# Kernel optimization log

Hardware: AMD Instinct MI355X
Metric: run time of the kernel (lower is better)

The kernel has to match this reference:

```python
import jax, jax.numpy as jnp
import numpy as np

N = 100000        # nodes
E = 3200000       # random edges (avg degree 32); self-loops added in reference
IN, HID, HEADS, OUT = 10, 32, 2, 4
NEG_SLOPE = 0.2   # PyG GATConv default leaky_relu slope


def setup_inputs() -> dict:
    key = jax.random.key(0)
    ks = jax.random.split(key, 16)
    s = 0.1
    return {
        "x": jax.random.normal(ks[0], (N, IN), jnp.float32),
        "edge_index": jax.random.randint(ks[1], (2, E), 0, N),
        "W1": jax.random.normal(ks[2], (IN, HEADS * HID), jnp.float32) * s,
        "a1s": jax.random.normal(ks[3], (HEADS, HID), jnp.float32) * s,
        "a1d": jax.random.normal(ks[4], (HEADS, HID), jnp.float32) * s,
        "b1": jnp.zeros((HEADS * HID,), jnp.float32),
        "W2": jax.random.normal(ks[5], (HEADS * HID, HEADS * HID), jnp.float32) * s,
        "a2s": jax.random.normal(ks[6], (HEADS, HID), jnp.float32) * s,
        "a2d": jax.random.normal(ks[7], (HEADS, HID), jnp.float32) * s,
        "b2": jnp.zeros((HEADS * HID,), jnp.float32),
        "W3": jax.random.normal(ks[8], (HEADS * HID, OUT), jnp.float32) * s,
        "a3s": jax.random.normal(ks[9], (1, OUT), jnp.float32) * s,
        "a3d": jax.random.normal(ks[10], (1, OUT), jnp.float32) * s,
        "b3": jnp.zeros((OUT,), jnp.float32),
    }


def gat_layer(x, src, dst, W, a_src, a_dst, b, concat):
    """One PyG-style GATConv (shared src/dst linear, self-loops already in src/dst)."""
    heads, oc = a_src.shape
    h = (x @ W).reshape(-1, heads, oc)                    # [N, H, C]
    asc = jnp.einsum('nhc,hc->nh', h, a_src)              # [N, H]
    adc = jnp.einsum('nhc,hc->nh', h, a_dst)              # [N, H]
    e = jax.nn.leaky_relu(asc[src] + adc[dst], NEG_SLOPE) # [Etot, H]
    m = jax.ops.segment_max(e, dst, num_segments=N)       # segment softmax over dst
    ex = jnp.exp(e - m[dst])
    z = jax.ops.segment_sum(ex, dst, num_segments=N)
    alpha = ex / z[dst]                                   # [Etot, H]
    out = jax.ops.segment_sum(h[src] * alpha[:, :, None], dst, num_segments=N)
    out = out.reshape(-1, heads * oc) if concat else out.mean(axis=1)
    return out + b


def reference(x, edge_index, W1, a1s, a1d, b1, W2, a2s, a2d, b2, W3, a3s, a3d, b3):
    loops = jnp.arange(N)
    src = jnp.concatenate([edge_index[0], loops])
    dst = jnp.concatenate([edge_index[1], loops])
    h = jax.nn.relu(gat_layer(x, src, dst, W1, a1s, a1d, b1, True))
    h = jax.nn.relu(gat_layer(h, src, dst, W2, a2s, a2d, b2, True))
    h = gat_layer(h, src, dst, W3, a3s, a3d, b3, False)
    return jax.nn.sigmoid(h) * 100.0
```

## Files before the change

kernel.cpp:

```cpp
#include <hip/hip_runtime.h>
#include <hip/hip_bf16.h>
#include <math.h>

#define NEG_SLOPE 0.2f
#define PSHIFT 8
#define PSIZE 256
#define NPARTS_MAX 392
#define B1 768
#define CELL_CAP 32
#define PCAP 10240
#define LCSR_CAP 10240

typedef int vint2 __attribute__((ext_vector_type(2)));
typedef int vint4 __attribute__((ext_vector_type(4)));
typedef short bf16x8 __attribute__((ext_vector_type(8)));
typedef float floatx4 __attribute__((ext_vector_type(4)));

__device__ __forceinline__ float lrelu(float v) { return fmaxf(v, NEG_SLOPE * v); }

__device__ __forceinline__ unsigned short f2bf(float f) {
    unsigned int b = __float_as_uint(f);
    b += 0x7fffu + ((b >> 16) & 1u);
    return (unsigned short)(b >> 16);
}

__global__ void k_part(const int* __restrict__ src, const int* __restrict__ dst, int E,
                       int* __restrict__ pairs, int* __restrict__ ptot, int nparts) {
    __shared__ int stage[NPARTS_MAX * CELL_CAP];
    __shared__ int lcnt[NPARTS_MAX];
    int tid = threadIdx.x, blk = blockIdx.x;
    for (int i = tid; i < nparts; i += 256) lcnt[i] = 0;
    __syncthreads();
    int per = ((E + B1 * 4 - 1) / (B1 * 4)) * 4;
    int s = blk * per, e = min(E, s + per);
    bool al = ((E & 3) == 0);
    for (int i0 = s + tid * 4; i0 < e; i0 += 1024) {
        int dv[4], sv[4], nv;
        if (al && i0 + 4 <= e) {
            vint4 d4 = __builtin_nontemporal_load((const vint4*)(dst + i0));
            vint4 s4 = __builtin_nontemporal_load((const vint4*)(src + i0));
            dv[0] = d4.x; dv[1] = d4.y; dv[2] = d4.z; dv[3] = d4.w;
            sv[0] = s4.x; sv[1] = s4.y; sv[2] = s4.z; sv[3] = s4.w;
            nv = 4;
        } else {
            nv = min(4, e - i0);
            for (int k = 0; k < nv; ++k) {
                dv[k] = __builtin_nontemporal_load(dst + i0 + k);
                sv[k] = __builtin_nontemporal_load(src + i0 + k);
            }
        }
        for (int k = 0; k < nv; ++k) {
            int p = dv[k] >> PSHIFT;
            int pos = atomicAdd(&lcnt[p], 1);
            if (pos < CELL_CAP)
                stage[p * CELL_CAP + pos] = (sv[k] << PSHIFT) | (dv[k] & (PSIZE - 1));
        }
    }
    __syncthreads();
    for (int p = tid; p < nparts; p += 256) {
        int tgt = min(lcnt[p], CELL_CAP);
        if (tgt == 0) continue;
        int base = atomicAdd(&ptot[p], tgt);
        if (base + tgt > PCAP) tgt = max(0, PCAP - base);
        int* gp = pairs + (size_t)p * PCAP + base;
        const int* sp = &stage[p * CELL_CAP];
        for (int j = 0; j < tgt; ++j) gp[j] = sp[j];
    }
}

__global__ void k_pscan(const int* __restrict__ ptot, int* __restrict__ pbase,
                        int* __restrict__ row, int nparts, int N) {
    __shared__ int sh[512];
    int tid = threadIdx.x;
    int v = (tid < nparts) ? min(ptot[tid], PCAP) : 0;
    sh[tid] = v;
    __syncthreads();
    for (int off = 1; off < 512; off <<= 1) {
        int t = (tid >= off) ? sh[tid - off] : 0;
        __syncthreads();
        sh[tid] += t;
        __syncthreads();
    }
    if (tid < nparts) pbase[tid] = sh[tid] - v;
    if (tid == nparts - 1) row[N] = sh[tid];
}

__global__ void k_scat2(const int* __restrict__ pairs, const int* __restrict__ ptot,
                        const int* __restrict__ pbase, int* __restrict__ row,
                        int* __restrict__ csr, int N) {
    __shared__ int lcsr[LCSR_CAP];
    __shared__ int lhist[PSIZE], lcur[PSIZE];
    int part = blockIdx.x;
    int lo = part << PSHIFT;
    int npart = min(PSIZE, N - lo);
    int tid = threadIdx.x;
    int cnt = min(ptot[part], PCAP);
    const int* seg = pairs + (size_t)part * PCAP;
    for (int i = tid; i < PSIZE; i += 1024) lhist[i] = 0;
    __syncthreads();
    for (int i = tid; i < cnt; i += 1024)
        atomicAdd(&lhist[__builtin_nontemporal_load(&seg[i]) & (PSIZE - 1)], 1);
    __syncthreads();
    if (tid < PSIZE) lcur[tid] = lhist[tid];
    __syncthreads();
    for (int off = 1; off < PSIZE; off <<= 1) {
        int t = 0;
        if (tid < PSIZE && tid >= off) t = lcur[tid - off];
        __syncthreads();
        if (tid < PSIZE) lcur[tid] += t;
        __syncthreads();
    }
    int pb = pbase[part];
    if (tid < npart) row[lo + tid] = pb + lcur[tid] - lhist[tid];
    if (tid < PSIZE) lcur[tid] -= lhist[tid];
    __syncthreads();
    for (int i = tid; i < cnt; i += 1024) {
        int v = __builtin_nontemporal_load(&seg[i]);
        int pos = atomicAdd(&lcur[v & (PSIZE - 1)], 1);
        if (pos < LCSR_CAP) lcsr[pos] = (unsigned)v >> PSHIFT;
    }
    __syncthreads();
    for (int i = tid; i < cnt; i += 1024)
        csr[pb + i] = lcsr[i];
}

__global__ void k_lin1(const float* __restrict__ x, const float* __restrict__ W,
                       const float* __restrict__ as_, const float* __restrict__ ad_,
                       unsigned short* __restrict__ hb, float* __restrict__ asc,
                       float* __restrict__ adc, int N) {
    __shared__ float sW[10 * 64];
    int tid = threadIdx.x;
    for (int i = tid; i < 640; i += 256) sW[i] = W[i];
    __syncthreads();
    int wid = tid >> 6, lane = tid & 63;
    int n = blockIdx.x * 4 + wid;
    if (n >= N) return;
    float acc = 0.f;
#pragma unroll
    for (int k = 0; k < 10; ++k) acc += x[n * 10 + k] * sW[k * 64 + lane];
    hb[(size_t)n * 64 + lane] = f2bf(acc);
    int head = lane >> 5, cc = lane & 31;
    float rs = acc * as_[lane];
    float rd = acc * ad_[lane];
#pragma unroll
    for (int m = 16; m >= 1; m >>= 1) {
        rs += __shfl_xor(rs, m, 64);
        rd += __shfl_xor(rd, m, 64);
    }
    if (cc == 0) { asc[n * 2 + head] = rs; adc[n * 2 + head] = rd; }
}

__global__ void k_lin2(const float* __restrict__ yin, const float* __restrict__ W,
                       const float* __restrict__ as_, const float* __restrict__ ad_,
                       unsigned short* __restrict__ hb, float* __restrict__ asc,
                       float* __restrict__ adc, int N) {
    __shared__ unsigned short sW[64 * 64];
    int tid = threadIdx.x;
    for (int i = tid; i < 4096; i += 256) sW[i] = f2bf(W[i]);
    __syncthreads();
    int wid = tid >> 6, lane = tid & 63;
    int quad = lane >> 4, col = lane & 15;
    bf16x8 bfr[4][2];
#pragma unroll
    for (int blk = 0; blk < 4; ++blk)
#pragma unroll
        for (int kh = 0; kh < 2; ++kh)
#pragma unroll
            for (int j = 0; j < 8; ++j)
                bfr[blk][kh][j] = (short)sW[(kh * 32 + quad * 8 + j) * 64 + blk * 16 + col];
    float asv[4], adv[4];
#pragma unroll
    for (int blk = 0; blk < 4; ++blk) {
        asv[blk] = as_[blk * 16 + col];
        adv[blk] = ad_[blk * 16 + col];
    }
    int tile = blockIdx.x * 4 + wid;
    int nb = tile * 16;
    if (nb >= N) return;
    int mrow = nb + col; if (mrow >= N) mrow = N - 1;
    const float* yr = yin + (size_t)mrow * 64;
    bf16x8 afr[2];
#pragma unroll
    for (int kh = 0; kh < 2; ++kh) {
        const float4* p = (const float4*)(yr + kh * 32 + quad * 8);
        float4 u0 = p[0], u1 = p[1];
        afr[kh][0] = (short)f2bf(u0.x); afr[kh][1] = (short)f2bf(u0.y);
        afr[kh][2] = (short)f2bf(u0.z); afr[kh][3] = (short)f2bf(u0.w);
        afr[kh][4] = (short)f2bf(u1.x); afr[kh][5] = (short)f2bf(u1.y);
        afr[kh][6] = (short)f2bf(u1.z); afr[kh][7] = (short)f2bf(u1.w);
    }
    floatx4 acc[4];
#pragma unroll
    for (int blk = 0; blk < 4; ++blk) {
        acc[blk][0] = 0.f; acc[blk][1] = 0.f; acc[blk][2] = 0.f; acc[blk][3] = 0.f;
        acc[blk] = __builtin_amdgcn_mfma_f32_16x16x32_bf16(afr[0], bfr[blk][0], acc[blk], 0, 0, 0);
        acc[blk] = __builtin_amdgcn_mfma_f32_16x16x32_bf16(afr[1], bfr[blk][1], acc[blk], 0, 0, 0);
    }
#pragma unroll
    for (int r = 0; r < 4; ++r) {
        int m = nb + quad * 4 + r;
        if (m < N) {
#pragma unroll
            for (int blk = 0; blk < 4; ++blk)
                hb[(size_t)m * 64 + blk * 16 + col] = f2bf(acc[blk][r]);
        }
    }
    float s0[4], s1[4], d0[4], d1[4];
#pragma unroll
    for (int r = 0; r < 4; ++r) {
        s0[r] = acc[0][r] * asv[0] + acc[1][r] * asv[1];
        s1[r] = acc[2][r] * asv[2] + acc[3][r] * asv[3];
        d0[r] = acc[0][r] * adv[0] + acc[1][r] * adv[1];
        d1[r] = acc[2][r] * adv[2] + acc[3][r] * adv[3];
    }
#pragma unroll
    for (int mask = 8; mask >= 1; mask >>= 1) {
#pragma unroll
        for (int r = 0; r < 4; ++r) {
            s0[r] += __shfl_xor(s0[r], mask, 64);
            s1[r] += __shfl_xor(s1[r], mask, 64);
            d0[r] += __shfl_xor(d0[r], mask, 64);
            d1[r] += __shfl_xor(d1[r], mask, 64);
        }
    }
    if (col < 4) {
        int m = nb + quad * 4 + col;
        if (m < N) {
            float vs0 = col == 0 ? s0[0] : col == 1 ? s0[1] : col == 2 ? s0[2] : s0[3];
            float vs1 = col == 0 ? s1[0] : col == 1 ? s1[1] : col == 2 ? s1[2] : s1[3];
            float vd0 = col == 0 ? d0[0] : col == 1 ? d0[1] : col == 2 ? d0[2] : d0[3];
            float vd1 = col == 0 ? d1[0] : col == 1 ? d1[1] : col == 2 ? d1[2] : d1[3];
            asc[m * 2 + 0] = vs0; asc[m * 2 + 1] = vs1;
            adc[m * 2 + 0] = vd0; adc[m * 2 + 1] = vd1;
        }
    }
}

__global__ void k_agg(const unsigned short* __restrict__ hb, const float* __restrict__ asc,
                      const float* __restrict__ adc, const int* __restrict__ row,
                      const int* __restrict__ csr_src, const float* __restrict__ bias,
                      float* __restrict__ yout, int N, int do_relu) {
    __shared__ vint2 tbl[4][64];
    int tid = threadIdx.x;
    int wid = tid >> 6, lane = tid & 63;
    int n = blockIdx.x * 4 + wid;
    if (n >= N) return;
    int s = row[n], e = row[n + 1];
    int chq = lane & 15;
    int hq = chq >> 3;
    int jo = lane >> 4;
    float2 ad = ((const float2*)adc)[n];
    float2 asf = ((const float2*)asc)[n];
    float p_self0 = __expf(lrelu(asf.x + ad.x));
    float p_self1 = __expf(lrelu(asf.y + ad.y));
    float z0a = (lane == 0) ? p_self0 : 0.f;
    float z1a = (lane == 0) ? p_self1 : 0.f;
    float a0 = 0.f, a1 = 0.f, a2 = 0.f, a3 = 0.f;
    const char* hbase = (const char*)hb;
    int choff = chq << 3;
    for (int base = s; base < e; base += 32) {
        int cnt = e - base; if (cnt > 32) cnt = 32;
        if (lane < 32) {
            int idx = base + lane;
            int srcv = 0;
            float p0 = 0.f, p1 = 0.f;
            if (idx < e) {
                srcv = csr_src[idx];
                float2 av = ((const float2*)asc)[srcv];
                p0 = __expf(lrelu(av.x + ad.x));
                p1 = __expf(lrelu(av.y + ad.y));
            }
            z0a += p0; z1a += p1;
            int boff = srcv << 7;
            vint2 e0; e0.x = boff; e0.y = __float_as_int(p0);
            vint2 e1; e1.x = boff; e1.y = __float_as_int(p1);
            tbl[wid][lane] = e0;
            tbl[wid][32 + lane] = e1;
        }
        __builtin_amdgcn_wave_barrier();
        int tb = hq << 5;
#pragma unroll 4
        for (int j = jo; j < cnt; j += 4) {
            vint2 t = tbl[wid][tb | j];
            vint2 pk = *(const vint2*)(hbase + (unsigned)t.x + choff);
            float p = __int_as_float(t.y);
            unsigned int pa = (unsigned int)pk.x, pb = (unsigned int)pk.y;
            a0 += p * __uint_as_float(pa << 16);
            a1 += p * __uint_as_float(pa & 0xffff0000u);
            a2 += p * __uint_as_float(pb << 16);
            a3 += p * __uint_as_float(pb & 0xffff0000u);
        }
        __builtin_amdgcn_wave_barrier();
    }
    a0 += __shfl_xor(a0, 16, 64); a1 += __shfl_xor(a1, 16, 64);
    a2 += __shfl_xor(a2, 16, 64); a3 += __shfl_xor(a3, 16, 64);
    a0 += __shfl_xor(a0, 32, 64); a1 += __shfl_xor(a1, 32, 64);
    a2 += __shfl_xor(a2, 32, 64); a3 += __shfl_xor(a3, 32, 64);
#pragma unroll
    for (int msk = 16; msk >= 1; msk >>= 1) {
        z0a += __shfl_xor(z0a, msk, 64);
        z1a += __shfl_xor(z1a, msk, 64);
    }
    z0a += __shfl_xor(z0a, 32, 64);
    z1a += __shfl_xor(z1a, 32, 64);
    float zneed = hq ? z1a : z0a;
    float p_self_my = hq ? p_self1 : p_self0;
    vint2 pks = *(const vint2*)(hbase + ((unsigned)n << 7) + choff);
    unsigned int sa = (unsigned int)pks.x, sb = (unsigned int)pks.y;
    a0 += p_self_my * __uint_as_float(sa << 16);
    a1 += p_self_my * __uint_as_float(sa & 0xffff0000u);
    a2 += p_self_my * __uint_as_float(sb << 16);
    a3 += p_self_my * __uint_as_float(sb & 0xffff0000u);
    float inv = 1.f / zneed;
    float4 bv = ((const float4*)bias)[chq];
    float y0 = a0 * inv + bv.x;
    float y1 = a1 * inv + bv.y;
    float y2 = a2 * inv + bv.z;
    float y3 = a3 * inv + bv.w;
    if (do_relu) {
        y0 = fmaxf(y0, 0.f); y1 = fmaxf(y1, 0.f);
        y2 = fmaxf(y2, 0.f); y3 = fmaxf(y3, 0.f);
    }
    if (lane < 16) {
        float4 o; o.x = y0; o.y = y1; o.z = y2; o.w = y3;
        ((float4*)yout)[(size_t)n * 16 + chq] = o;
    }
}

__global__ void k_lin3(const float* __restrict__ yin, const float* __restrict__ W3,
                       const float* __restrict__ a3s, const float* __restrict__ a3d,
                       float4* __restrict__ rec, int N) {
    __shared__ float sW[256];
    int tid = threadIdx.x;
    sW[tid] = W3[tid];
    __syncthreads();
    int t = blockIdx.x * 256 + tid;
    int n = t >> 2, c = t & 3;
    if (n >= N) return;
    float acc = 0.f;
#pragma unroll
    for (int k = 0; k < 64; ++k) acc += yin[(size_t)n * 64 + k] * sW[k * 4 + c];
    float rs = acc * a3s[c], rd = acc * a3d[c];
    rs += __shfl_xor(rs, 1, 64); rs += __shfl_xor(rs, 2, 64);
    rd += __shfl_xor(rd, 1, 64); rd += __shfl_xor(rd, 2, 64);
    float a_1 = __shfl_xor(acc, 1, 64);
    float a_2 = __shfl_xor(acc, 2, 64);
    float a_3 = __shfl_xor(acc, 3, 64);
    if (c == 0) {
        unsigned int lo = (unsigned int)f2bf(acc) | ((unsigned int)f2bf(a_1) << 16);
        unsigned int hi = (unsigned int)f2bf(a_2) | ((unsigned int)f2bf(a_3) << 16);
        float4 r;
        r.x = __uint_as_float(lo); r.y = __uint_as_float(hi);
        r.z = rs; r.w = rd;
        rec[n] = r;
    }
}

__global__ void k_agg3(const float4* __restrict__ rec, const int* __restrict__ row,
                       const int* __restrict__ csr_src, const float* __restrict__ b3,
                       float* __restrict__ out, int N) {
    int tid = threadIdx.x;
    int wid = tid >> 6, lane = tid & 63;
    int n = blockIdx.x * 4 + wid;
    if (n >= N) return;
    int s = row[n], e = row[n + 1];
    float4 rn = rec[n];
    float adcn = rn.w;
    float n0 = 0.f, n1 = 0.f, n2 = 0.f, n3 = 0.f, den = 0.f;
    if (lane == 0) {
        float p = __expf(lrelu(rn.z + adcn));
        unsigned int lo = __float_as_uint(rn.x), hi = __float_as_uint(rn.y);
        n0 = p * __uint_as_float(lo << 16);
        n1 = p * __uint_as_float(lo & 0xffff0000u);
        n2 = p * __uint_as_float(hi << 16);
        n3 = p * __uint_as_float(hi & 0xffff0000u);
        den = p;
    }
    for (int idx = s + lane; idx < e; idx += 64) {
        int src = csr_src[idx];
        float4 r = rec[src];
        float p = __expf(lrelu(r.z + adcn));
        unsigned int lo = __float_as_uint(r.x), hi = __float_as_uint(r.y);
        n0 += p * __uint_as_float(lo << 16);
        n1 += p * __uint_as_float(lo & 0xffff0000u);
        n2 += p * __uint_as_float(hi << 16);
        n3 += p * __uint_as_float(hi & 0xffff0000u);
        den += p;
    }
#pragma unroll
    for (int msk = 32; msk >= 1; msk >>= 1) {
        n0 += __shfl_xor(n0, msk, 64);
        n1 += __shfl_xor(n1, msk, 64);
        n2 += __shfl_xor(n2, msk, 64);
        n3 += __shfl_xor(n3, msk, 64);
        den += __shfl_xor(den, msk, 64);
    }
    if (lane < 4) {
        float num = lane == 0 ? n0 : lane == 1 ? n1 : lane == 2 ? n2 : n3;
        float v = num / den + b3[lane];
        out[n * 4 + lane] = 100.f / (1.f + __expf(-v));
    }
}

extern "C" void kernel_launch(void* const* d_in, const int* in_sizes, int n_in,
                              void* d_out, int out_size, void* d_ws, size_t ws_size,
                              hipStream_t stream) {
    const float* x   = (const float*)d_in[0];
    const int*   ei  = (const int*)d_in[1];
    const float* W1  = (const float*)d_in[2];
    const float* a1s = (const float*)d_in[3];
    const float* a1d = (const float*)d_in[4];
    const float* b1  = (const float*)d_in[5];
    const float* W2  = (const float*)d_in[6];
    const float* a2s = (const float*)d_in[7];
    const float* a2d = (const float*)d_in[8];
    const float* b2  = (const float*)d_in[9];
    const float* W3  = (const float*)d_in[10];
    const float* a3s = (const float*)d_in[11];
    const float* a3d = (const float*)d_in[12];
    const float* b3  = (const float*)d_in[13];
    float* out = (float*)d_out;

    const int N = in_sizes[0] / 10;
    const int E = in_sizes[1] / 2;
    const int* esrc = ei;
    const int* edst = ei + E;
    const int nparts = (N + PSIZE - 1) >> PSHIFT;

    char* ws = (char*)d_ws;
    size_t off = 0;
    auto alloc = [&](size_t bytes) {
        void* p = ws + off;
        off = (off + bytes + 255) & ~(size_t)255;
        return p;
    };
    int*   row   = (int*)alloc((size_t)(N + 1) * sizeof(int));
    int*   ptot  = (int*)alloc(NPARTS_MAX * sizeof(int));
    int*   pbase = (int*)alloc(NPARTS_MAX * sizeof(int));
    int*   csr   = (int*)alloc((size_t)E * sizeof(int));
    unsigned short* hb = (unsigned short*)alloc((size_t)N * 64 * sizeof(unsigned short));
    float* y     = (float*)alloc((size_t)N * 64 * sizeof(float));
    float4* rec  = (float4*)alloc((size_t)N * sizeof(float4));
    float* asc   = (float*)alloc((size_t)N * 2 * sizeof(float));
    float* adc   = (float*)alloc((size_t)N * 2 * sizeof(float));
    int* pairs = (int*)hb;

    (void)hipMemsetAsync(ptot, 0, NPARTS_MAX * sizeof(int), stream);

    const int nw = (N + 3) / 4;
    const int tiles = (N + 15) / 16;

    k_part<<<B1, 256, 0, stream>>>(esrc, edst, E, pairs, ptot, nparts);
    k_pscan<<<1, 512, 0, stream>>>(ptot, pbase, row, nparts, N);
    k_scat2<<<nparts, 1024, 0, stream>>>(pairs, ptot, pbase, row, csr, N);

    k_lin1<<<nw, 256, 0, stream>>>(x, W1, a1s, a1d, hb, asc, adc, N);
    k_agg<<<nw, 256, 0, stream>>>(hb, asc, adc, row, csr, b1, y, N, 1);
    k_lin2<<<(tiles + 3) / 4, 256, 0, stream>>>(y, W2, a2s, a2d, hb, asc, adc, N);
    k_agg<<<nw, 256, 0, stream>>>(hb, asc, adc, row, csr, b2, y, N, 1);
    k_lin3<<<(N * 4 + 255) / 256, 256, 0, stream>>>(y, W3, a3s, a3d, rec, N);
    k_agg3<<<nw, 256, 0, stream>>>(rec, row, csr, b3, out, N);
}
```

Before: 362.8 us.

## Fuse partition with layer-1 linear, inline prefix scan, widen agg loads

Merges the edge-partitioning pass and the layer-1 linear transform into one launch by giving extra blocks the linear work. The partition staging buffer moves from hb to y so the two can run together. The separate partition prefix-scan kernel is removed; every scatter block now recomputes the 512-entry scan redundantly. The aggregation kernel now has each lane load 16 bytes (8 bf16 channels) per neighbor with 8 edges in flight instead of 4, which cuts launch count and per-edge instruction overhead but raises register use.

```diff
diff --git a/kernel.cpp b/kernel.cpp
--- a/kernel.cpp
+++ b/kernel.cpp
@@ -24,77 +24,98 @@
     return (unsigned short)(b >> 16);
 }
 
-__global__ void k_part(const int* __restrict__ src, const int* __restrict__ dst, int E,
-                       int* __restrict__ pairs, int* __restrict__ ptot, int nparts) {
-    __shared__ int stage[NPARTS_MAX * CELL_CAP];
+__global__ void k_build(const int* __restrict__ src, const int* __restrict__ dst, int E,
+                        int* __restrict__ pairs, int* __restrict__ ptot, int nparts,
+                        const float* __restrict__ x, const float* __restrict__ W,
+                        const float* __restrict__ as_, const float* __restrict__ ad_,
+                        unsigned short* __restrict__ hb, float* __restrict__ asc,
+                        float* __restrict__ adc, int N) {
+    __shared__ int shmem[NPARTS_MAX * CELL_CAP];
     __shared__ int lcnt[NPARTS_MAX];
-    int tid = threadIdx.x, blk = blockIdx.x;
-    for (int i = tid; i < nparts; i += 256) lcnt[i] = 0;
-    __syncthreads();
-    int per = ((E + B1 * 4 - 1) / (B1 * 4)) * 4;
-    int s = blk * per, e = min(E, s + per);
-    bool al = ((E & 3) == 0);
-    for (int i0 = s + tid * 4; i0 < e; i0 += 1024) {
-        int dv[4], sv[4], nv;
-        if (al && i0 + 4 <= e) {
-            vint4 d4 = __builtin_nontemporal_load((const vint4*)(dst + i0));
-            vint4 s4 = __builtin_nontemporal_load((const vint4*)(src + i0));
-            dv[0] = d4.x; dv[1] = d4.y; dv[2] = d4.z; dv[3] = d4.w;
-            sv[0] = s4.x; sv[1] = s4.y; sv[2] = s4.z; sv[3] = s4.w;
-            nv = 4;
-        } else {
-            nv = min(4, e - i0);
+    int tid = threadIdx.x;
+    if (blockIdx.x < B1) {
+        int blk = blockIdx.x;
+        for (int i = tid; i < nparts; i += 256) lcnt[i] = 0;
+        __syncthreads();
+        int per = ((E + B1 * 4 - 1) / (B1 * 4)) * 4;
+        int s = blk * per, e = min(E, s + per);
+        bool al = ((E & 3) == 0);
+        for (int i0 = s + tid * 4; i0 < e; i0 += 1024) {
+            int dv[4], sv[4], nv;
+            if (al && i0 + 4 <= e) {
+                vint4 d4 = __builtin_nontemporal_load((const vint4*)(dst + i0));
+                vint4 s4 = __builtin_nontemporal_load((const vint4*)(src + i0));
+                dv[0] = d4.x; dv[1] = d4.y; dv[2] = d4.z; dv[3] = d4.w;
+                sv[0] = s4.x; sv[1] = s4.y; sv[2] = s4.z; sv[3] = s4.w;
+                nv = 4;
+            } else {
+                nv = min(4, e - i0);
+                for (int k = 0; k < nv; ++k) {
+                    dv[k] = __builtin_nontemporal_load(dst + i0 + k);
+                    sv[k] = __builtin_nontemporal_load(src + i0 + k);
+                }
+            }
             for (int k = 0; k < nv; ++k) {
-                dv[k] = __builtin_nontemporal_load(dst + i0 + k);
-                sv[k] = __builtin_nontemporal_load(src + i0 + k);
+                int p = dv[k] >> PSHIFT;
+                int pos = atomicAdd(&lcnt[p], 1);
+                if (pos < CELL_CAP)
+                    shmem[p * CELL_CAP + pos] = (sv[k] << PSHIFT) | (dv[k] & (PSIZE - 1));
             }
         }
-        for (int k = 0; k < nv; ++k) {
-            int p = dv[k] >> PSHIFT;
-            int pos = atomicAdd(&lcnt[p], 1);
-            if (pos < CELL_CAP)
-                stage[p * CELL_CAP + pos] = (sv[k] << PSHIFT) | (dv[k] & (PSIZE - 1));
-        }
-    }
-    __syncthreads();
-    for (int p = tid; p < nparts; p += 256) {
-        int tgt = min(lcnt[p], CELL_CAP);
-        if (tgt == 0) continue;
-        int base = atomicAdd(&ptot[p], tgt);
-        if (base + tgt > PCAP) tgt = max(0, PCAP - base);
-        int* gp = pairs + (size_t)p * PCAP + base;
-        const int* sp = &stage[p * CELL_CAP];
-        for (int j = 0; j < tgt; ++j) gp[j] = sp[j];
-    }
-}
-
-__global__ void k_pscan(const int* __restrict__ ptot, int* __restrict__ pbase,
-                        int* __restrict__ row, int nparts, int N) {
-    __shared__ int sh[512];
-    int tid = threadIdx.x;
-    int v = (tid < nparts) ? min(ptot[tid], PCAP) : 0;
-    sh[tid] = v;
-    __syncthreads();
-    for (int off = 1; off < 512; off <<= 1) {
-        int t = (tid >= off) ? sh[tid - off] : 0;
-        __syncthreads();
-        sh[tid] += t;
-        __syncthreads();
-    }
-    if (tid < nparts) pbase[tid] = sh[tid] - v;
-    if (tid == nparts - 1) row[N] = sh[tid];
+        __syncthreads();
+        for (int p = tid; p < nparts; p += 256) {
+            int tgt = min(lcnt[p], CELL_CAP);
+            if (tgt == 0) continue;
+            int base = atomicAdd(&ptot[p], tgt);
+            if (base + tgt > PCAP) tgt = max(0, PCAP - base);
+            int* gp = pairs + (size_t)p * PCAP + base;
+            const int* sp = &shmem[p * CELL_CAP];
+            for (int j = 0; j < tgt; ++j) gp[j] = sp[j];
+        }
+    } else {
+        float* sW = (float*)shmem;
+        for (int i = tid; i < 640; i += 256) sW[i] = W[i];
+        __syncthreads();
+        int wid = tid >> 6, lane = tid & 63;
+        int n = (blockIdx.x - B1) * 4 + wid;
+        if (n >= N) return;
+        float acc = 0.f;
+#pragma unroll
+        for (int k = 0; k < 10; ++k) acc += x[n * 10 + k] * sW[k * 64 + lane];
+        hb[(size_t)n * 64 + lane] = f2bf(acc);
+        int head = lane >> 5, cc = lane & 31;
+        float rs = acc * as_[lane];
+        float rd = acc * ad_[lane];
+#pragma unroll
+        for (int m = 16; m >= 1; m >>= 1) {
+            rs += __shfl_xor(rs, m, 64);
+            rd += __shfl_xor(rd, m, 64);
+        }
+        if (cc == 0) { asc[n * 2 + head] = rs; adc[n * 2 + head] = rd; }
+    }
 }
 
 __global__ void k_scat2(const int* __restrict__ pairs, const int* __restrict__ ptot,
-                        const int* __restrict__ pbase, int* __restrict__ row,
-                        int* __restrict__ csr, int N) {
+                        int* __restrict__ row, int* __restrict__ csr, int N, int nparts) {
     __shared__ int lcsr[LCSR_CAP];
     __shared__ int lhist[PSIZE], lcur[PSIZE];
+    __shared__ int sscan[512];
     int part = blockIdx.x;
     int lo = part << PSHIFT;
     int npart = min(PSIZE, N - lo);
     int tid = threadIdx.x;
+    if (tid < 512) sscan[tid] = (tid < nparts) ? min(ptot[tid], PCAP) : 0;
+    __syncthreads();
+    for (int off = 1; off < 512; off <<= 1) {
+        int t = 0;
+        if (tid < 512 && tid >= off) t = sscan[tid - off];
+        __syncthreads();
+        if (tid < 512) sscan[tid] += t;
+        __syncthreads();
+    }
     int cnt = min(ptot[part], PCAP);
+    int pb = sscan[part] - cnt;
+    if (part == 0 && tid == 0) row[N] = sscan[nparts - 1];
     const int* seg = pairs + (size_t)part * PCAP;
     for (int i = tid; i < PSIZE; i += 1024) lhist[i] = 0;
     __syncthreads();
@@ -110,7 +131,6 @@
         if (tid < PSIZE) lcur[tid] += t;
         __syncthreads();
     }
-    int pb = pbase[part];
     if (tid < npart) row[lo + tid] = pb + lcur[tid] - lhist[tid];
     if (tid < PSIZE) lcur[tid] -= lhist[tid];
     __syncthreads();
@@ -122,32 +142,6 @@
     __syncthreads();
     for (int i = tid; i < cnt; i += 1024)
         csr[pb + i] = lcsr[i];
-}
-
-__global__ void k_lin1(const float* __restrict__ x, const float* __restrict__ W,
-                       const float* __restrict__ as_, const float* __restrict__ ad_,
-                       unsigned short* __restrict__ hb, float* __restrict__ asc,
-                       float* __restrict__ adc, int N) {
-    __shared__ float sW[10 * 64];
-    int tid = threadIdx.x;
-    for (int i = tid; i < 640; i += 256) sW[i] = W[i];
-    __syncthreads();
-    int wid = tid >> 6, lane = tid & 63;
-    int n = blockIdx.x * 4 + wid;
-    if (n >= N) return;
-    float acc = 0.f;
-#pragma unroll
-    for (int k = 0; k < 10; ++k) acc += x[n * 10 + k] * sW[k * 64 + lane];
-    hb[(size_t)n * 64 + lane] = f2bf(acc);
-    int head = lane >> 5, cc = lane & 31;
-    float rs = acc * as_[lane];
-    float rd = acc * ad_[lane];
-#pragma unroll
-    for (int m = 16; m >= 1; m >>= 1) {
-        rs += __shfl_xor(rs, m, 64);
-        rd += __shfl_xor(rd, m, 64);
-    }
-    if (cc == 0) { asc[n * 2 + head] = rs; adc[n * 2 + head] = rd; }
 }
 
 __global__ void k_lin2(const float* __restrict__ yin, const float* __restrict__ W,
@@ -246,9 +240,9 @@
     int n = blockIdx.x * 4 + wid;
     if (n >= N) return;
     int s = row[n], e = row[n + 1];
-    int chq = lane & 15;
-    int hq = chq >> 3;
-    int jo = lane >> 4;
+    int chq = lane & 7;
+    int hq = chq >> 2;
+    int jo = lane >> 3;
     float2 ad = ((const float2*)adc)[n];
     float2 asf = ((const float2*)asc)[n];
     float p_self0 = __expf(lrelu(asf.x + ad.x));
@@ -256,8 +250,9 @@
     float z0a = (lane == 0) ? p_self0 : 0.f;
     float z1a = (lane == 0) ? p_self1 : 0.f;
     float a0 = 0.f, a1 = 0.f, a2 = 0.f, a3 = 0.f;
+    float a4 = 0.f, a5 = 0.f, a6 = 0.f, a7 = 0.f;
     const char* hbase = (const char*)hb;
-    int choff = chq << 3;
+    int choff = chq << 4;
     for (int base = s; base < e; base += 32) {
         int cnt = e - base; if (cnt > 32) cnt = 32;
         if (lane < 32) {
@@ -280,22 +275,30 @@
         __builtin_amdgcn_wave_barrier();
         int tb = hq << 5;
 #pragma unroll 4
-        for (int j = jo; j < cnt; j += 4) {
+        for (int j = jo; j < cnt; j += 8) {
             vint2 t = tbl[wid][tb | j];
-            vint2 pk = *(const vint2*)(hbase + (unsigned)t.x + choff);
+            vint4 pk = *(const vint4*)(hbase + (unsigned)t.x + choff);
             float p = __int_as_float(t.y);
-            unsigned int pa = (unsigned int)pk.x, pb = (unsigned int)pk.y;
-            a0 += p * __uint_as_float(pa << 16);
-            a1 += p * __uint_as_float(pa & 0xffff0000u);
-            a2 += p * __uint_as_float(pb << 16);
-            a3 += p * __uint_as_float(pb & 0xffff0000u);
+            unsigned int w0 = (unsigned int)pk.x, w1 = (unsigned int)pk.y;
+            unsigned int w2 = (unsigned int)pk.z, w3 = (unsigned int)pk.w;
+            a0 += p * __uint_as_float(w0 << 16);
+            a1 += p * __uint_as_float(w0 & 0xffff0000u);
+            a2 += p * __uint_as_float(w1 << 16);
+            a3 += p * __uint_as_float(w1 & 0xffff0000u);
+            a4 += p * __uint_as_float(w2 << 16);
+            a5 += p * __uint_as_float(w2 & 0xffff0000u);
+            a6 += p * __uint_as_float(w3 << 16);
+            a7 += p * __uint_as_float(w3 & 0xffff0000u);
         }
         __builtin_amdgcn_wave_barrier();
     }
-    a0 += __shfl_xor(a0, 16, 64); a1 += __shfl_xor(a1, 16, 64);
-    a2 += __shfl_xor(a2, 16, 64); a3 += __shfl_xor(a3, 16, 64);
-    a0 += __shfl_xor(a0, 32, 64); a1 += __shfl_xor(a1, 32, 64);
-    a2 += __shfl_xor(a2, 32, 64); a3 += __shfl_xor(a3, 32, 64);
+#pragma unroll
+    for (int msk = 8; msk <= 32; msk <<= 1) {
+        a0 += __shfl_xor(a0, msk, 64); a1 += __shfl_xor(a1, msk, 64);
+        a2 += __shfl_xor(a2, msk, 64); a3 += __shfl_xor(a3, msk, 64);
+        a4 += __shfl_xor(a4, msk, 64); a5 += __shfl_xor(a5, msk, 64);
+        a6 += __shfl_xor(a6, msk, 64); a7 += __shfl_xor(a7, msk, 64);
+    }
 #pragma unroll
     for (int msk = 16; msk >= 1; msk >>= 1) {
         z0a += __shfl_xor(z0a, msk, 64);
@@ -305,25 +308,34 @@
     z1a += __shfl_xor(z1a, 32, 64);
     float zneed = hq ? z1a : z0a;
     float p_self_my = hq ? p_self1 : p_self0;
-    vint2 pks = *(const vint2*)(hbase + ((unsigned)n << 7) + choff);
-    unsigned int sa = (unsigned int)pks.x, sb = (unsigned int)pks.y;
-    a0 += p_self_my * __uint_as_float(sa << 16);
-    a1 += p_self_my * __uint_as_float(sa & 0xffff0000u);
-    a2 += p_self_my * __uint_as_float(sb << 16);
-    a3 += p_self_my * __uint_as_float(sb & 0xffff0000u);
+    vint4 pks = *(const vint4*)(hbase + ((unsigned)n << 7) + choff);
+    unsigned int s0 = (unsigned int)pks.x, s1 = (unsigned int)pks.y;
+    unsigned int s2 = (unsigned int)pks.z, s3 = (unsigned int)pks.w;
+    a0 += p_self_my * __uint_as_float(s0 << 16);
+    a1 += p_self_my * __uint_as_float(s0 & 0xffff0000u);
+    a2 += p_self_my * __uint_as_float(s1 << 16);
+    a3 += p_self_my * __uint_as_float(s1 & 0xffff0000u);
+    a4 += p_self_my * __uint_as_float(s2 << 16);
+    a5 += p_self_my * __uint_as_float(s2 & 0xffff0000u);
+    a6 += p_self_my * __uint_as_float(s3 << 16);
+    a7 += p_self_my * __uint_as_float(s3 & 0xffff0000u);
     float inv = 1.f / zneed;
-    float4 bv = ((const float4*)bias)[chq];
-    float y0 = a0 * inv + bv.x;
-    float y1 = a1 * inv + bv.y;
-    float y2 = a2 * inv + bv.z;
-    float y3 = a3 * inv + bv.w;
+    float4 bv0 = ((const float4*)bias)[chq * 2];
+    float4 bv1 = ((const float4*)bias)[chq * 2 + 1];
+    float4 o0, o1;
+    o0.x = a0 * inv + bv0.x; o0.y = a1 * inv + bv0.y;
+    o0.z = a2 * inv + bv0.z; o0.w = a3 * inv + bv0.w;
+    o1.x = a4 * inv + bv1.x; o1.y = a5 * inv + bv1.y;
+    o1.z = a6 * inv + bv1.z; o1.w = a7 * inv + bv1.w;
     if (do_relu) {
-        y0 = fmaxf(y0, 0.f); y1 = fmaxf(y1, 0.f);
-        y2 = fmaxf(y2, 0.f); y3 = fmaxf(y3, 0.f);
-    }
-    if (lane < 16) {
-        float4 o; o.x = y0; o.y = y1; o.z = y2; o.w = y3;
-        ((float4*)yout)[(size_t)n * 16 + chq] = o;
+        o0.x = fmaxf(o0.x, 0.f); o0.y = fmaxf(o0.y, 0.f);
+        o0.z = fmaxf(o0.z, 0.f); o0.w = fmaxf(o0.w, 0.f);
+        o1.x = fmaxf(o1.x, 0.f); o1.y = fmaxf(o1.y, 0.f);
+        o1.z = fmaxf(o1.z, 0.f); o1.w = fmaxf(o1.w, 0.f);
+    }
+    if (lane < 8) {
+        ((float4*)yout)[(size_t)n * 16 + chq * 2] = o0;
+        ((float4*)yout)[(size_t)n * 16 + chq * 2 + 1] = o1;
     }
 }
 
@@ -436,25 +448,23 @@
     };
     int*   row   = (int*)alloc((size_t)(N + 1) * sizeof(int));
     int*   ptot  = (int*)alloc(NPARTS_MAX * sizeof(int));
-    int*   pbase = (int*)alloc(NPARTS_MAX * sizeof(int));
     int*   csr   = (int*)alloc((size_t)E * sizeof(int));
     unsigned short* hb = (unsigned short*)alloc((size_t)N * 64 * sizeof(unsigned short));
     float* y     = (float*)alloc((size_t)N * 64 * sizeof(float));
     float4* rec  = (float4*)alloc((size_t)N * sizeof(float4));
     float* asc   = (float*)alloc((size_t)N * 2 * sizeof(float));
     float* adc   = (float*)alloc((size_t)N * 2 * sizeof(float));
-    int* pairs = (int*)hb;
+    int* pairs = (int*)y;
 
     (void)hipMemsetAsync(ptot, 0, NPARTS_MAX * sizeof(int), stream);
 
     const int nw = (N + 3) / 4;
     const int tiles = (N + 15) / 16;
 
-    k_part<<<B1, 256, 0, stream>>>(esrc, edst, E, pairs, ptot, nparts);
-    k_pscan<<<1, 512, 0, stream>>>(ptot, pbase, row, nparts, N);
-    k_scat2<<<nparts, 1024, 0, stream>>>(pairs, ptot, pbase, row, csr, N);
-
-    k_lin1<<<nw, 256, 0, stream>>>(x, W1, a1s, a1d, hb, asc, adc, N);
+    k_build<<<B1 + nw, 256, 0, stream>>>(esrc, edst, E, pairs, ptot, nparts,
+                                         x, W1, a1s, a1d, hb, asc, adc, N);
+    k_scat2<<<nparts, 1024, 0, stream>>>(pairs, ptot, row, csr, N, nparts);
+
     k_agg<<<nw, 256, 0, stream>>>(hb, asc, adc, row, csr, b1, y, N, 1);
     k_lin2<<<(tiles + 3) / 4, 256, 0, stream>>>(y, W2, a2s, a2d, hb, asc, adc, N);
     k_agg<<<nw, 256, 0, stream>>>(hb, asc, adc, row, csr, b2, y, N, 1);
```

Measured after the change: 382.8 us. +5.5%, slower.
